# Kernel optimization log

Hardware: AMD Instinct MI355X
Metric: run time of the kernel (lower is better)

## Reference

```python
import jax, jax.numpy as jnp
import numpy as np

L, H, P = 16384, 1024, 512  # seq_len, features, state size


def setup_inputs() -> dict:
    key = jax.random.key(0)
    ks = jax.random.split(key, 7)
    input_sequence = jax.random.normal(ks[0], (L, H), dtype=jnp.float32)
    # Stable diagonal state matrix: real part strictly negative (left half plane)
    Lambda_re = -0.5 * jax.random.uniform(ks[1], (P,), dtype=jnp.float32) - 1e-2
    Lambda_im = 3.0 * jax.random.normal(ks[2], (P,), dtype=jnp.float32)
    # B_tilde = B_ri[...,0] + 1j*B_ri[...,1], shape (P, H); lecun-ish scale
    B_ri = jax.random.normal(ks[3], (P, H, 2), dtype=jnp.float32) / np.sqrt(H)
    # bidirectional: C_tilde has 2P columns (concat of C1, C2)
    C_ri = jax.random.normal(ks[4], (H, 2 * P, 2), dtype=jnp.float32) / np.sqrt(2 * P)
    D = jax.random.normal(ks[5], (H,), dtype=jnp.float32)
    log_step = jax.random.uniform(ks[6], (P,), dtype=jnp.float32,
                                  minval=np.log(1e-3).astype(np.float32),
                                  maxval=np.log(1e-1).astype(np.float32))
    return dict(input_sequence=input_sequence, Lambda_re=Lambda_re,
                Lambda_im=Lambda_im, B_ri=B_ri, C_ri=C_ri, D=D,
                log_step=log_step)


def _binop(ei, ej):
    # associative operator for diagonal linear recurrence x_t = a_t*x_{t-1} + bu_t
    a_i, bu_i = ei
    a_j, bu_j = ej
    return a_i * a_j, a_j * bu_i + bu_j


def reference(input_sequence, Lambda_re, Lambda_im, B_ri, C_ri, D, log_step):
    u = input_sequence  # (L, H) real
    Lam = Lambda_re + 1j * Lambda_im              # (P,) complex
    B_tilde = B_ri[..., 0] + 1j * B_ri[..., 1]    # (P, H) complex
    C_tilde = C_ri[..., 0] + 1j * C_ri[..., 1]    # (H, 2P) complex
    step = jnp.exp(log_step)                      # (P,), step_rescale = 1.0
    # ZOH discretization
    Lambda_bar = jnp.exp(step * Lam)              # (P,)
    B_bar = ((Lambda_bar - 1.0) / Lam)[:, None] * B_tilde  # (P, H)
    # Bu_t = B_bar @ u_t for all t, vectorized as one GEMM: (L,H)@(H,P) -> (L,P)
    Bu = u.astype(B_bar.dtype) @ B_bar.T          # (L, P) complex
    A = jnp.broadcast_to(Lambda_bar, (u.shape[0], Lam.shape[0]))  # (L, P)
    _, xs_f = jax.lax.associative_scan(_binop, (A, Bu))
    _, xs_b = jax.lax.associative_scan(_binop, (A, Bu), reverse=True)
    xs = jnp.concatenate([xs_f, xs_b], axis=1)    # (L, 2P) complex
    # conj_sym=True -> output is 2 * Re(C_tilde @ x)
    ys = 2.0 * (xs @ C_tilde.T).real              # (L, H) real
    return ys + D * u
```

## Files before the change

### kernel.cpp

```cpp
#include <hip/hip_runtime.h>
#include <cstdint>
#include <cmath>

#define L_SEQ 16384
#define H_DIM 1024
#define P_DIM 512
#define NCH   256
#define RCH   64

typedef short short4v __attribute__((ext_vector_type(4)));
typedef short short8v __attribute__((ext_vector_type(8)));
typedef float f32x4   __attribute__((ext_vector_type(4)));

__device__ __forceinline__ unsigned short f2bf(float f) {
    unsigned int u = __float_as_uint(f);
    u += 0x7FFFu + ((u >> 16) & 1u);
    return (unsigned short)(u >> 16);
}

#define GLD16(gp, lp) __builtin_amdgcn_global_load_lds( \
    (const __attribute__((address_space(1))) void*)(gp), \
    (__attribute__((address_space(3))) void*)(lp), 16, 0, 0)

#define VMCNT6 asm volatile("s_waitcnt vmcnt(6)" ::: "memory")
#define VMCNT0 asm volatile("s_waitcnt vmcnt(0)" ::: "memory")
#define BARRIER do { asm volatile("" ::: "memory"); \
                     __builtin_amdgcn_s_barrier(); \
                     asm volatile("" ::: "memory"); } while (0)

__device__ __forceinline__ void lam_pow(const float* Lre, const float* Lim,
                                        const float* lstep, int p, float tmul,
                                        float& ar, float& ai) {
    float step = expf(lstep[p]) * tmul;
    float lr = Lre[p], li = Lim[p];
    float mag = expf(step * lr);
    float ang = step * li;
    ar = mag * cosf(ang);
    ai = mag * sinf(ang);
}


__global__ void conv_u(const float* __restrict__ u, short* __restrict__ ub) {
    size_t i = ((size_t)blockIdx.x * 256 + threadIdx.x) * 8;
    const float4* s = (const float4*)(u + i);
    float4 v0 = s[0], v1 = s[1];
    short8v o;
    o[0] = (short)f2bf(v0.x); o[1] = (short)f2bf(v0.y);
    o[2] = (short)f2bf(v0.z); o[3] = (short)f2bf(v0.w);
    o[4] = (short)f2bf(v1.x); o[5] = (short)f2bf(v1.y);
    o[6] = (short)f2bf(v1.z); o[7] = (short)f2bf(v1.w);
    *(short8v*)&ub[i] = o;
}

__global__ void prep_B(const float* __restrict__ B_ri, short* __restrict__ Bcat,
                       const float* Lre, const float* Lim, const float* lstep) {
    int t = blockIdx.x * 256 + threadIdx.x;
    int p  = t >> 8;
    int h4 = (t & 255) << 2;
    float step = expf(lstep[p]);
    float lr = Lre[p], li = Lim[p];
    float mag = expf(step * lr);
    float cr = mag * cosf(step * li) - 1.0f;
    float ci = mag * sinf(step * li);
    float den = lr * lr + li * li;
    float sr = (cr * lr + ci * li) / den;
    float si = (ci * lr - cr * li) / den;
    const float4* src = (const float4*)(B_ri + ((size_t)p * H_DIM + h4) * 2);
    float4 v0 = src[0], v1 = src[1];
    short4v re, im;
    re[0] = (short)f2bf(sr * v0.x - si * v0.y); im[0] = (short)f2bf(sr * v0.y + si * v0.x);
    re[1] = (short)f2bf(sr * v0.z - si * v0.w); im[1] = (short)f2bf(sr * v0.w + si * v0.z);
    re[2] = (short)f2bf(sr * v1.x - si * v1.y); im[2] = (short)f2bf(sr * v1.y + si * v1.x);
    re[3] = (short)f2bf(sr * v1.z - si * v1.w); im[3] = (short)f2bf(sr * v1.w + si * v1.z);
    *(short4v*)&Bcat[(size_t)p * H_DIM + h4] = re;
    *(short4v*)&Bcat[(size_t)(p + P_DIM) * H_DIM + h4] = im;
}

__global__ void prep_C(const float* __restrict__ C_ri, short* __restrict__ Ccat) {
    int t = blockIdx.x * 256 + threadIdx.x;
    int h  = t >> 8;
    int c4 = (t & 255) << 2;
    const float4* src = (const float4*)(C_ri + ((size_t)h * 1024 + c4) * 2);
    float4 v0 = src[0], v1 = src[1];
    short4v re, im;
    re[0] = (short)f2bf(2.0f * v0.x); im[0] = (short)f2bf(-2.0f * v0.y);
    re[1] = (short)f2bf(2.0f * v0.z); im[1] = (short)f2bf(-2.0f * v0.w);
    re[2] = (short)f2bf(2.0f * v1.x); im[2] = (short)f2bf(-2.0f * v1.y);
    re[3] = (short)f2bf(2.0f * v1.z); im[3] = (short)f2bf(-2.0f * v1.w);
    *(short4v*)&Ccat[(size_t)h * 2048 + c4] = re;
    *(short4v*)&Ccat[(size_t)h * 2048 + 1024 + c4] = im;
}


__global__ void scan_phase_a(const float* __restrict__ Bu, float* __restrict__ E,
                             const float* Lre, const float* Lim, const float* lstep) {
    int chunk = blockIdx.x, dir = blockIdx.y;
    int j = threadIdx.x;
    float ar, ai; lam_pow(Lre, Lim, lstep, j, 1.0f, ar, ai);
    float xr = 0.f, xi = 0.f;
    int base = chunk * RCH;
    for (int i = 0; i < RCH; ++i) {
        int row = dir ? (base + RCH - 1 - i) : (base + i);
        float br = Bu[(size_t)row * 1024 + j];
        float bi = Bu[(size_t)row * 1024 + P_DIM + j];
        float nr = fmaf(ar, xr, fmaf(-ai, xi, br));
        float ni = fmaf(ar, xi, fmaf( ai, xr, bi));
        xr = nr; xi = ni;
    }
    size_t o = ((size_t)dir * NCH + chunk) * 1024 + j;
    E[o] = xr; E[o + P_DIM] = xi;
}

__global__ void carry_seg(const float* __restrict__ E, float* __restrict__ G,
                          const float* Lre, const float* Lim, const float* lstep) {
    int s = blockIdx.x, dir = blockIdx.y, j = threadIdx.x;
    float ar, ai; lam_pow(Lre, Lim, lstep, j, (float)RCH, ar, ai);
    float gr = 0.f, gi = 0.f;
    for (int t = 0; t < 16; ++t) {
        int pos = s * 16 + t;
        int c = dir ? (NCH - 1 - pos) : pos;
        size_t o = ((size_t)dir * NCH + c) * 1024 + j;
        float er = E[o], ei = E[o + P_DIM];
        float nr = fmaf(ar, gr, fmaf(-ai, gi, er));
        float ni = fmaf(ar, gi, fmaf( ai, gr, ei));
        gr = nr; gi = ni;
    }
    size_t o = ((size_t)dir * 16 + s) * 1024 + j;
    G[o] = gr; G[o + P_DIM] = gi;
}

__global__ void carry_mid(const float* __restrict__ G, float* __restrict__ T,
                          const float* Lre, const float* Lim, const float* lstep) {
    int dir = blockIdx.x, j = threadIdx.x;
    float ar, ai; lam_pow(Lre, Lim, lstep, j, (float)(RCH * 16), ar, ai);
    float tr = 0.f, ti = 0.f;
    for (int s = 0; s < 16; ++s) {
        size_t o = ((size_t)dir * 16 + s) * 1024 + j;
        T[o] = tr; T[o + P_DIM] = ti;
        float gr = G[o], gi = G[o + P_DIM];
        float nr = fmaf(ar, tr, fmaf(-ai, ti, gr));
        float ni = fmaf(ar, ti, fmaf( ai, tr, gi));
        tr = nr; ti = ni;
    }
}

__global__ void carry_exp(const float* __restrict__ E, const float* __restrict__ T,
                          float* __restrict__ S,
                          const float* Lre, const float* Lim, const float* lstep) {
    int s = blockIdx.x, dir = blockIdx.y, j = threadIdx.x;
    float ar, ai; lam_pow(Lre, Lim, lstep, j, (float)RCH, ar, ai);
    size_t ot = ((size_t)dir * 16 + s) * 1024 + j;
    float xr = T[ot], xi = T[ot + P_DIM];
    for (int t = 0; t < 16; ++t) {
        int pos = s * 16 + t;
        int c = dir ? (NCH - 1 - pos) : pos;
        size_t o = ((size_t)dir * NCH + c) * 1024 + j;
        S[o] = xr; S[o + P_DIM] = xi;
        float er = E[o], ei = E[o + P_DIM];
        float nr = fmaf(ar, xr, fmaf(-ai, xi, er));
        float ni = fmaf(ar, xi, fmaf( ai, xr, ei));
        xr = nr; xi = ni;
    }
}

__global__ void scan_phase_c(const float* __restrict__ Bu, const float* __restrict__ S,
                             short* __restrict__ XS,
                             const float* Lre, const float* Lim, const float* lstep) {
    int chunk = blockIdx.x, dir = blockIdx.y;
    int j = threadIdx.x;
    float ar, ai; lam_pow(Lre, Lim, lstep, j, 1.0f, ar, ai);
    size_t so = ((size_t)dir * NCH + chunk) * 1024 + j;
    float xr = S[so], xi = S[so + P_DIM];
    int base = chunk * RCH;
    int reo = dir ? (P_DIM + j) : j;
    int imo = reo + 1024;
    for (int i = 0; i < RCH; ++i) {
        int row = dir ? (base + RCH - 1 - i) : (base + i);
        float br = Bu[(size_t)row * 1024 + j];
        float bi = Bu[(size_t)row * 1024 + P_DIM + j];
        float nr = fmaf(ar, xr, fmaf(-ai, xi, br));
        float ni = fmaf(ar, xi, fmaf( ai, xr, bi));
        xr = nr; xi = ni;
        XS[(size_t)row * 2048 + reo] = (short)f2bf(xr);
        XS[(size_t)row * 2048 + imo] = (short)f2bf(xi);
    }
}

#define SUB(b,op,kh) (&lds[((((b)*2)+(op))*2+(kh))*8192])

#define LDB(base) do { const short* _p = (base); \
    b0 = *(const short8v*)&_p[roffB];        b1 = *(const short8v*)&_p[roffB + 512]; \
    b2 = *(const short8v*)&_p[roffB + 1024]; b3 = *(const short8v*)&_p[roffB + 1536]; } while (0)
#define LDAL(base) do { const short* _p = (base); \
    aL0 = *(const short8v*)&_p[roffA];        aL1 = *(const short8v*)&_p[roffA + 512]; \
    aL2 = *(const short8v*)&_p[roffA + 1024]; aL3 = *(const short8v*)&_p[roffA + 1536]; } while (0)
#define LDAH(base) do { const short* _p = (base); \
    aH0 = *(const short8v*)&_p[roffA + 2048]; aH1 = *(const short8v*)&_p[roffA + 2560]; \
    aH2 = *(const short8v*)&_p[roffA + 3072]; aH3 = *(const short8v*)&_p[roffA + 3584]; } while (0)

#define MF4(mi, a) \
    acc[mi][0] = __builtin_amdgcn_mfma_f32_16x16x32_bf16(a, b0, acc[mi][0], 0,0,0); \
    acc[mi][1] = __builtin_amdgcn_mfma_f32_16x16x32_bf16(a, b1, acc[mi][1], 0,0,0); \
    acc[mi][2] = __builtin_amdgcn_mfma_f32_16x16x32_bf16(a, b2, acc[mi][2], 0,0,0); \
    acc[mi][3] = __builtin_amdgcn_mfma_f32_16x16x32_bf16(a, b3, acc[mi][3], 0,0,0);

#define MFMA16L do { __builtin_amdgcn_s_setprio(1); \
    MF4(0, aL0) MF4(1, aL1) MF4(2, aL2) MF4(3, aL3) \
    __builtin_amdgcn_s_setprio(0); } while (0)
#define MFMA16H do { __builtin_amdgcn_s_setprio(1); \
    MF4(4, aH0) MF4(5, aH1) MF4(6, aH2) MF4(7, aH3) \
    __builtin_amdgcn_s_setprio(0); } while (0)

template<int M, int N, int K, bool EPI>
__global__ __launch_bounds__(512, 2) void gemm2r(
    const short* __restrict__ A, const short* __restrict__ Bm, float* __restrict__ Co,
    const float* __restrict__ Dv, const float* __restrict__ U)
{
    __shared__ __align__(16) short lds[65536];
    constexpr int NTN = N / 256;
    constexpr int nwg = (M / 256) * NTN;
    constexpr int NT  = K / 64;
    static_assert(nwg % 8 == 0, "bijective XCD swizzle");

    int tid = threadIdx.x;
    int wave = tid >> 6, lane = tid & 63;
    int bid = blockIdx.x;
    int wg  = (bid & 7) * (nwg / 8) + (bid >> 3);
    int m0 = (wg / NTN) * 256, n0 = (wg % NTN) * 256;
    int wm = (wave >> 2) * 128, wn = (wave & 3) * 64;
    int lr = lane & 15;
    int sA = (lane >> 4) ^ ((lane >> 1) & 3);
    int roffA = (wm + lr) * 32 + sA * 8;
    int roffB = (wn + lr) * 32 + sA * 8;

    const short* Ag = A  + (size_t)m0 * K;
    const short* Bg = Bm + (size_t)n0 * K;

    int sl0 = tid, sl1 = 512 + tid;
    size_t ga0 = (size_t)(sl0 >> 2) * K + (size_t)((((sl0 & 3) ^ ((sl0 >> 3) & 3))) * 8);
    size_t ga1 = (size_t)(sl1 >> 2) * K + (size_t)((((sl1 & 3) ^ ((sl1 >> 3) & 3))) * 8);
    int ld0 = sl0 * 8, ld1 = sl1 * 8;

    f32x4 acc[8][4];
#pragma unroll
    for (int m = 0; m < 8; ++m)
#pragma unroll
        for (int n = 0; n < 4; ++n) acc[m][n] = (f32x4){0.f, 0.f, 0.f, 0.f};

#define STAGE(G, k0, sb) do { short* _s = (sb); \
        GLD16((G) + ga0 + (k0), &_s[ld0]); \
        GLD16((G) + ga1 + (k0), &_s[ld1]); } while (0)

    STAGE(Ag, 0,  SUB(0,0,0));
    STAGE(Bg, 0,  SUB(0,1,0));
    STAGE(Ag, 32, SUB(0,0,1));
    STAGE(Bg, 32, SUB(0,1,1));

    short8v aL0, aL1, aL2, aL3, aH0, aH1, aH2, aH3, b0, b1, b2, b3;

    for (int t = 0; t < NT; ++t) {
        int b = t & 1, nb = b ^ 1;
        int kn = ((t + 1 < NT) ? (t + 1) : 0) * 64;
        const short* Ab0 = SUB(b,0,0); const short* Ab1 = SUB(b,0,1);
        const short* Bb0 = SUB(b,1,0); const short* Bb1 = SUB(b,1,1);

        STAGE(Ag, kn, SUB(nb,0,0));
        VMCNT6;
        BARRIER;
        LDB(Bb0); LDAL(Ab0); LDAH(Ab0);
        MFMA16L;
        STAGE(Bg, kn, SUB(nb,1,0));
        MFMA16H;

        STAGE(Ag, kn + 32, SUB(nb,0,1));
        VMCNT6;
        BARRIER;
        LDB(Bb1); LDAL(Ab1); LDAH(Ab1);
        MFMA16L;
        STAGE(Bg, kn + 32, SUB(nb,1,1));
        MFMA16H;
    }
    VMCNT0;

    int lr4 = (lane >> 4) * 4;
#pragma unroll
    for (int m = 0; m < 8; ++m)
#pragma unroll
        for (int n = 0; n < 4; ++n) {
            int r = m0 + wm + m * 16 + lr4;
            int c = n0 + wn + n * 16 + lr;
#pragma unroll
            for (int i = 0; i < 4; ++i) {
                float v = acc[m][n][i];
                if constexpr (EPI)
                    v = fmaf(Dv[c], U[(size_t)(r + i) * N + c], v);
                Co[(size_t)(r + i) * N + c] = v;
            }
        }
#undef STAGE
}


extern "C" void kernel_launch(void* const* d_in, const int* in_sizes, int n_in,
                              void* d_out, int out_size, void* d_ws, size_t ws_size,
                              hipStream_t stream) {
    const float* u     = (const float*)d_in[0];
    const float* Lre   = (const float*)d_in[1];
    const float* Lim   = (const float*)d_in[2];
    const float* B_ri  = (const float*)d_in[3];
    const float* C_ri  = (const float*)d_in[4];
    const float* Dv    = (const float*)d_in[5];
    const float* lstep = (const float*)d_in[6];
    float* out = (float*)d_out;

    char* w = (char*)d_ws;
    short* u_bf = (short*)(w);
    short* XS   = (short*)(w);
    float* Gseg = (float*)(w + (33ull  << 20));
    float* Tseg = (float*)(w + (34ull  << 20));
    short* Bcat = (short*)(w + (64ull  << 20));
    float* Bu   = (float*)(w + (66ull  << 20));
    short* Ccat = (short*)(w + (130ull << 20));
    float* E    = (float*)(w + (134ull << 20));
    float* Scar = (float*)(w + (136ull << 20));

    conv_u<<<(L_SEQ * H_DIM) / (256 * 8), 256, 0, stream>>>(u, u_bf);
    prep_B<<<(P_DIM * H_DIM) / (256 * 4), 256, 0, stream>>>(B_ri, Bcat, Lre, Lim, lstep);
    prep_C<<<(H_DIM * 1024) / (256 * 4), 256, 0, stream>>>(C_ri, Ccat);

    gemm2r<L_SEQ, 1024, H_DIM, false><<<(L_SEQ / 256) * (1024 / 256), 512, 0, stream>>>(
        u_bf, Bcat, Bu, nullptr, nullptr);

    scan_phase_a<<<dim3(NCH, 2), P_DIM, 0, stream>>>(Bu, E, Lre, Lim, lstep);
    carry_seg<<<dim3(16, 2), P_DIM, 0, stream>>>(E, Gseg, Lre, Lim, lstep);
    carry_mid<<<2, P_DIM, 0, stream>>>(Gseg, Tseg, Lre, Lim, lstep);
    carry_exp<<<dim3(16, 2), P_DIM, 0, stream>>>(E, Tseg, Scar, Lre, Lim, lstep);
    scan_phase_c<<<dim3(NCH, 2), P_DIM, 0, stream>>>(Bu, Scar, XS, Lre, Lim, lstep);

    gemm2r<L_SEQ, H_DIM, 2048, true><<<(L_SEQ / 256) * (H_DIM / 256), 512, 0, stream>>>(
        XS, Ccat, out, Dv, u);
}
```

Before: 302.3 us.

## Store Bu in bf16, fuse bidirectional chunk-sum pass, restructure GEMM pipeline phases

The first GEMM now writes Bu as bf16 instead of fp32, halving its write traffic and the read traffic of both scan passes. Scan phase A computes the forward and backward chunk sums in one pass, using a running power of Lambda for the reverse direction, so Bu is read once instead of twice. The GEMM main loop is split into four phases, each with explicit LDS waits and extra barriers around the MFMA groups, and the vmcnt threshold changes. Risks are precision loss in Bu and extra barrier stalls in the GEMM.

Result: faster. 279.4 us (-7.6%).

```diff
diff --git a/kernel.cpp b/kernel.cpp
--- a/kernel.cpp
+++ b/kernel.cpp
@@ -17,13 +17,19 @@
     u += 0x7FFFu + ((u >> 16) & 1u);
     return (unsigned short)(u >> 16);
 }
+__device__ __forceinline__ float bf2f(short s) {
+    unsigned int u = ((unsigned int)(unsigned short)s) << 16;
+    return __uint_as_float(u);
+}
 
 #define GLD16(gp, lp) __builtin_amdgcn_global_load_lds( \
     (const __attribute__((address_space(1))) void*)(gp), \
     (__attribute__((address_space(3))) void*)(lp), 16, 0, 0)
 
-#define VMCNT6 asm volatile("s_waitcnt vmcnt(6)" ::: "memory")
+#define VMCNT4 asm volatile("s_waitcnt vmcnt(4)" ::: "memory")
 #define VMCNT0 asm volatile("s_waitcnt vmcnt(0)" ::: "memory")
+#define LGKM0  do { asm volatile("s_waitcnt lgkmcnt(0)" ::: "memory"); \
+                    __builtin_amdgcn_sched_barrier(0); } while (0)
 #define BARRIER do { asm volatile("" ::: "memory"); \
                      __builtin_amdgcn_s_barrier(); \
                      asm volatile("" ::: "memory"); } while (0)
@@ -92,23 +98,32 @@
 }
 
 
-__global__ void scan_phase_a(const float* __restrict__ Bu, float* __restrict__ E,
+__global__ void scan_phase_a(const short* __restrict__ Bu, float* __restrict__ E,
                              const float* Lre, const float* Lim, const float* lstep) {
-    int chunk = blockIdx.x, dir = blockIdx.y;
+    int chunk = blockIdx.x;
     int j = threadIdx.x;
     float ar, ai; lam_pow(Lre, Lim, lstep, j, 1.0f, ar, ai);
-    float xr = 0.f, xi = 0.f;
+    float fr = 0.f, fi = 0.f;
+    float gr = 0.f, gi = 0.f;
+    float wr = 1.f, wi = 0.f;
     int base = chunk * RCH;
     for (int i = 0; i < RCH; ++i) {
-        int row = dir ? (base + RCH - 1 - i) : (base + i);
-        float br = Bu[(size_t)row * 1024 + j];
-        float bi = Bu[(size_t)row * 1024 + P_DIM + j];
-        float nr = fmaf(ar, xr, fmaf(-ai, xi, br));
-        float ni = fmaf(ar, xi, fmaf( ai, xr, bi));
-        xr = nr; xi = ni;
-    }
-    size_t o = ((size_t)dir * NCH + chunk) * 1024 + j;
-    E[o] = xr; E[o + P_DIM] = xi;
+        int row = base + i;
+        float xr = bf2f(Bu[(size_t)row * 1024 + j]);
+        float xi = bf2f(Bu[(size_t)row * 1024 + P_DIM + j]);
+        float nfr = fmaf(ar, fr, fmaf(-ai, fi, xr));
+        float nfi = fmaf(ar, fi, fmaf( ai, fr, xi));
+        fr = nfr; fi = nfi;
+        gr = fmaf(wr, xr, fmaf(-wi, xi, gr));
+        gi = fmaf(wr, xi, fmaf( wi, xr, gi));
+        float nwr = wr * ar - wi * ai;
+        float nwi = wr * ai + wi * ar;
+        wr = nwr; wi = nwi;
+    }
+    size_t of = ((size_t)0 * NCH + chunk) * 1024 + j;
+    size_t ob = ((size_t)1 * NCH + chunk) * 1024 + j;
+    E[of] = fr; E[of + P_DIM] = fi;
+    E[ob] = gr; E[ob + P_DIM] = gi;
 }
 
 __global__ void carry_seg(const float* __restrict__ E, float* __restrict__ G,
@@ -163,7 +178,7 @@
     }
 }
 
-__global__ void scan_phase_c(const float* __restrict__ Bu, const float* __restrict__ S,
+__global__ void scan_phase_c(const short* __restrict__ Bu, const float* __restrict__ S,
                              short* __restrict__ XS,
                              const float* Lre, const float* Lim, const float* lstep) {
     int chunk = blockIdx.x, dir = blockIdx.y;
@@ -176,8 +191,8 @@
     int imo = reo + 1024;
     for (int i = 0; i < RCH; ++i) {
         int row = dir ? (base + RCH - 1 - i) : (base + i);
-        float br = Bu[(size_t)row * 1024 + j];
-        float bi = Bu[(size_t)row * 1024 + P_DIM + j];
+        float br = bf2f(Bu[(size_t)row * 1024 + j]);
+        float bi = bf2f(Bu[(size_t)row * 1024 + P_DIM + j]);
         float nr = fmaf(ar, xr, fmaf(-ai, xi, br));
         float ni = fmaf(ar, xi, fmaf( ai, xr, bi));
         xr = nr; xi = ni;
@@ -211,9 +226,9 @@
     MF4(4, aH0) MF4(5, aH1) MF4(6, aH2) MF4(7, aH3) \
     __builtin_amdgcn_s_setprio(0); } while (0)
 
-template<int M, int N, int K, bool EPI>
-__global__ __launch_bounds__(512, 2) void gemm2r(
-    const short* __restrict__ A, const short* __restrict__ Bm, float* __restrict__ Co,
+template<int M, int N, int K, int OUT>
+__global__ __launch_bounds__(512, 2) void gemm4p(
+    const short* __restrict__ A, const short* __restrict__ Bm, void* __restrict__ Co,
     const float* __restrict__ Dv, const float* __restrict__ U)
 {
     __shared__ __align__(16) short lds[65536];
@@ -255,6 +270,8 @@
     STAGE(Bg, 0,  SUB(0,1,0));
     STAGE(Ag, 32, SUB(0,0,1));
     STAGE(Bg, 32, SUB(0,1,1));
+    VMCNT4;
+    BARRIER;
 
     short8v aL0, aL1, aL2, aL3, aH0, aH1, aH2, aH3, b0, b1, b2, b3;
 
@@ -264,21 +281,35 @@
         const short* Ab0 = SUB(b,0,0); const short* Ab1 = SUB(b,0,1);
         const short* Bb0 = SUB(b,1,0); const short* Bb1 = SUB(b,1,1);
 
+        LDB(Bb0); LDAL(Ab0);
         STAGE(Ag, kn, SUB(nb,0,0));
-        VMCNT6;
-        BARRIER;
-        LDB(Bb0); LDAL(Ab0); LDAH(Ab0);
+        BARRIER;
+        LGKM0;
         MFMA16L;
+        BARRIER;
+
+        LDAH(Ab0);
         STAGE(Bg, kn, SUB(nb,1,0));
+        VMCNT4;
+        BARRIER;
+        LGKM0;
         MFMA16H;
-
+        BARRIER;
+
+        LDB(Bb1); LDAL(Ab1);
         STAGE(Ag, kn + 32, SUB(nb,0,1));
-        VMCNT6;
-        BARRIER;
-        LDB(Bb1); LDAL(Ab1); LDAH(Ab1);
+        BARRIER;
+        LGKM0;
         MFMA16L;
+        BARRIER;
+
+        LDAH(Ab1);
         STAGE(Bg, kn + 32, SUB(nb,1,1));
+        VMCNT4;
+        BARRIER;
+        LGKM0;
         MFMA16H;
+        BARRIER;
     }
     VMCNT0;
 
@@ -292,9 +323,12 @@
 #pragma unroll
             for (int i = 0; i < 4; ++i) {
                 float v = acc[m][n][i];
-                if constexpr (EPI)
+                if constexpr (OUT == 1) {
                     v = fmaf(Dv[c], U[(size_t)(r + i) * N + c], v);
-                Co[(size_t)(r + i) * N + c] = v;
+                    ((float*)Co)[(size_t)(r + i) * N + c] = v;
+                } else {
+                    ((short*)Co)[(size_t)(r + i) * N + c] = (short)f2bf(v);
+                }
             }
         }
 #undef STAGE
@@ -319,7 +353,7 @@
     float* Gseg = (float*)(w + (33ull  << 20));
     float* Tseg = (float*)(w + (34ull  << 20));
     short* Bcat = (short*)(w + (64ull  << 20));
-    float* Bu   = (float*)(w + (66ull  << 20));
+    short* Bu   = (short*)(w + (66ull  << 20));
     short* Ccat = (short*)(w + (130ull << 20));
     float* E    = (float*)(w + (134ull << 20));
     float* Scar = (float*)(w + (136ull << 20));
@@ -328,15 +362,15 @@
     prep_B<<<(P_DIM * H_DIM) / (256 * 4), 256, 0, stream>>>(B_ri, Bcat, Lre, Lim, lstep);
     prep_C<<<(H_DIM * 1024) / (256 * 4), 256, 0, stream>>>(C_ri, Ccat);
 
-    gemm2r<L_SEQ, 1024, H_DIM, false><<<(L_SEQ / 256) * (1024 / 256), 512, 0, stream>>>(
+    gemm4p<L_SEQ, 1024, H_DIM, 0><<<(L_SEQ / 256) * (1024 / 256), 512, 0, stream>>>(
         u_bf, Bcat, Bu, nullptr, nullptr);
 
-    scan_phase_a<<<dim3(NCH, 2), P_DIM, 0, stream>>>(Bu, E, Lre, Lim, lstep);
+    scan_phase_a<<<NCH, P_DIM, 0, stream>>>(Bu, E, Lre, Lim, lstep);
     carry_seg<<<dim3(16, 2), P_DIM, 0, stream>>>(E, Gseg, Lre, Lim, lstep);
     carry_mid<<<2, P_DIM, 0, stream>>>(Gseg, Tseg, Lre, Lim, lstep);
     carry_exp<<<dim3(16, 2), P_DIM, 0, stream>>>(E, Tseg, Scar, Lre, Lim, lstep);
     scan_phase_c<<<dim3(NCH, 2), P_DIM, 0, stream>>>(Bu, Scar, XS, Lre, Lim, lstep);
 
-    gemm2r<L_SEQ, H_DIM, 2048, true><<<(L_SEQ / 256) * (H_DIM / 256), 512, 0, stream>>>(
+    gemm4p<L_SEQ, H_DIM, 2048, 1><<<(L_SEQ / 256) * (H_DIM / 256), 512, 0, stream>>>(
         XS, Ccat, out, Dv, u);
 }
```
